# Optimization experiments

Hardware: AMD Instinct MI355X
Metric: run time of the kernel (lower is better)

The kernel has to match this reference:

```python
import jax, jax.numpy as jnp
import numpy as np

T, N, E, D = 6, 50000, 250000, 256   # edge types, nodes/type, edges/type, feat dim
H, C, K = 4, 64, 64                  # heads, head dim, diffpool clusters (H*C == D)
SCALE = 0.06


def setup_inputs():
    key = jax.random.key(0)
    ks = jax.random.split(key, 14)
    return {
        'x_pkg': jax.random.normal(ks[0], (N, D), jnp.float32),
        'x_dst': jax.random.normal(ks[1], (T, N, D), jnp.float32),
        'edge_index': jax.random.randint(ks[2], (T, 2, E), 0, N, jnp.int32),
        'edge_attr': jax.random.uniform(ks[3], (T, E, 1), jnp.float32),
        'node_mask': jnp.ones((N,), jnp.float32),
        'edge_mask': jax.random.uniform(ks[4], (E,), jnp.float32),
        'W1_src': jax.random.normal(ks[5], (T, D, H, C), jnp.float32) * SCALE,
        'W1_dst': jax.random.normal(ks[6], (T, D, H, C), jnp.float32) * SCALE,
        'a1': jax.random.normal(ks[7], (T, H, C), jnp.float32) * SCALE,
        'W2_src': jax.random.normal(ks[8], (T, D, H, C), jnp.float32) * SCALE,
        'W2_dst': jax.random.normal(ks[9], (T, D, H, C), jnp.float32) * SCALE,
        'a2': jax.random.normal(ks[10], (T, H, C), jnp.float32) * SCALE,
        'W_assign': jax.random.normal(ks[11], (D, K), jnp.float32) * SCALE,
        'W_cls': jax.random.normal(ks[12], (D + T, 1), jnp.float32) * SCALE,
        'b_cls': jnp.zeros((1,), jnp.float32),
    }


def _gatv2(x_src, x_dst, src, dst, Ws, Wd, a, edge_w):
    """GATv2Conv (bipartite, no self loops) with soft edge-mask weighting."""
    hs = jnp.einsum('nd,dhc->nhc', x_src, Ws)          # [N,H,C]
    hd = jnp.einsum('nd,dhc->nhc', x_dst, Wd)          # [N,H,C]
    hj = hs[src]                                        # [E,H,C] gathered source msgs
    e = jnp.sum(a * jax.nn.leaky_relu(hd[dst] + hj, 0.2), axis=-1)  # [E,H]
    m = jax.ops.segment_max(e, dst, num_segments=N)
    m = jnp.where(jnp.isfinite(m), m, 0.0)              # nodes with no in-edges
    p = jnp.exp(e - m[dst])
    den = jax.ops.segment_sum(p, dst, num_segments=N)
    alpha = p / (den[dst] + 1e-16)                      # softmax over in-neighbors
    msg = (alpha * edge_w[:, None])[:, :, None] * hj    # [E,H,C]
    return jax.ops.segment_sum(msg, dst, num_segments=N).reshape(N, H * C)


def reference(x_pkg, x_dst, edge_index, edge_attr, node_mask, edge_mask,
              W1_src, W1_dst, a1, W2_src, W2_dst, a2, W_assign, W_cls, b_cls):
    nm = node_mask[:, None]
    xm_pkg = x_pkg * nm
    # layer 1: hetero GATv2 per edge type (Package_Name -> dst type)
    h1 = [
        _gatv2(xm_pkg, x_dst[t] * nm, edge_index[t, 0], edge_index[t, 1],
               W1_src[t], W1_dst[t], a1[t], edge_mask)
        for t in range(T)
    ]
    # layer 2 on relu'd features (H*C == D so dims line up)
    x2_src = jax.nn.relu(x_pkg)
    h2 = [
        _gatv2(x2_src, jax.nn.relu(h1[t]), edge_index[t, 0], edge_index[t, 1],
               W2_src[t], W2_dst[t], a2[t], edge_mask)
        for t in range(T)
    ]
    # diffpool on last processed node type
    x_last = h2[-1]                                     # [N, D]
    S = jax.nn.softmax(x_last @ W_assign, axis=-1)      # [N, K] cluster assignment
    x_pool = S.T @ x_last                               # [K, D]
    # global aggregated edge features (mean per edge type)
    agg_edge = jnp.concatenate([edge_attr[t].mean(axis=0) for t in range(T)], -1)  # [T]
    feats = jnp.concatenate([x_pool, jnp.broadcast_to(agg_edge, (K, T))], axis=-1)
    logits = feats @ W_cls + b_cls                      # [K, 1]
    return jax.nn.sigmoid(logits)
```

## Files before the change

kernel.cpp:

```cpp
#include <hip/hip_runtime.h>
#include <math.h>

#define NN 50000
#define EE 250000
#define TTT 6
#define DD 256
#define HH 4
#define CC 64
#define KDIM 64

typedef __bf16 bf16x4 __attribute__((ext_vector_type(4)));
typedef __bf16 bf16x8 __attribute__((ext_vector_type(8)));
typedef float  f32x4  __attribute__((ext_vector_type(4)));

__device__ __forceinline__ void mfma_bf16(f32x4& d, bf16x8 a, bf16x8 b) {
    asm("v_mfma_f32_16x16x32_bf16 %0, %1, %2, %0" : "+v"(d) : "v"(a), "v"(b));
}

__global__ __launch_bounds__(256) void prep_b_k(
    const float* __restrict__ B0, const float* __restrict__ B1,
    const float* __restrict__ B2, const float* __restrict__ B3,
    __bf16* __restrict__ outp)
{
    int w = blockIdx.y;
    const float* B = (w == 0) ? B0 : (w == 1) ? B1 : (w == 2) ? B2 : B3;
    __bf16* oh = outp + (size_t)w * 2 * DD * DD;
    __bf16* ol = oh + DD * DD;
    int i = blockIdx.x * 256 + threadIdx.x;
    int k = i >> 8, n = i & 255;
    float x = B[i];
    __bf16 h = (__bf16)x;
    __bf16 l = (__bf16)(x - (float)h);
    oh[(size_t)n * DD + k] = h;
    ol[(size_t)n * DD + k] = l;
}

#define BM 128
#define BN 128
#define BK 64

__global__ __launch_bounds__(256, 2) void gemm_mfma_k(
    const float* __restrict__ A, const __bf16* __restrict__ Bt,
    float* __restrict__ Cout, const float* __restrict__ rowscale,
    int op, int nrows)
{
    __shared__ __align__(16) __bf16 Ah[BM * BK], Al[BM * BK];
    __shared__ __align__(16) __bf16 Bh[BN * BK], Bl[BN * BK];
    const __bf16* Bth = Bt;
    const __bf16* Btl = Bt + DD * DD;
    int tid = threadIdx.x;
    int row0 = blockIdx.x * BM;
    int col0 = blockIdx.y * BN;
    int lane = tid & 63;
    int wv = tid >> 6;
    int wm = (wv >> 1) * 64;
    int wn = (wv & 1) * 64;
    f32x4 acc[4][4] = {};

    for (int k0 = 0; k0 < DD; k0 += BK) {
        #pragma unroll
        for (int li = 0; li < 8; ++li) {
            int i = tid + li * 256;
            int r = i >> 4;
            int kq = (i & 15) * 4;
            int gr = row0 + r;
            float4 v = make_float4(0.f, 0.f, 0.f, 0.f);
            if (gr < nrows) {
                v = *(const float4*)&A[(size_t)gr * DD + k0 + kq];
                if (op == 0) {
                    float s = rowscale[gr];
                    v.x *= s; v.y *= s; v.z *= s; v.w *= s;
                } else {
                    v.x = fmaxf(v.x, 0.f); v.y = fmaxf(v.y, 0.f);
                    v.z = fmaxf(v.z, 0.f); v.w = fmaxf(v.w, 0.f);
                }
            }
            bf16x4 hv, lv;
            hv[0] = (__bf16)v.x; hv[1] = (__bf16)v.y;
            hv[2] = (__bf16)v.z; hv[3] = (__bf16)v.w;
            lv[0] = (__bf16)(v.x - (float)hv[0]);
            lv[1] = (__bf16)(v.y - (float)hv[1]);
            lv[2] = (__bf16)(v.z - (float)hv[2]);
            lv[3] = (__bf16)(v.w - (float)hv[3]);
            int kk = kq ^ ((r & 7) << 3);
            *(bf16x4*)&Ah[r * BK + kk] = hv;
            *(bf16x4*)&Al[r * BK + kk] = lv;
        }
        #pragma unroll
        for (int li = 0; li < 4; ++li) {
            int i = tid + li * 256;
            int r = i >> 3;
            int kc = (i & 7) * 8;
            int kk = kc ^ ((r & 7) << 3);
            *(bf16x8*)&Bh[r * BK + kk] = *(const bf16x8*)&Bth[(size_t)(col0 + r) * DD + k0 + kc];
            *(bf16x8*)&Bl[r * BK + kk] = *(const bf16x8*)&Btl[(size_t)(col0 + r) * DD + k0 + kc];
        }
        __syncthreads();
        #pragma unroll
        for (int ks = 0; ks < 2; ++ks) {
            bf16x8 af[4], alf[4], bfr[4], blf[4];
            int kb = ks * 32 + (lane >> 4) * 8;
            #pragma unroll
            for (int i2 = 0; i2 < 4; ++i2) {
                int r = wm + i2 * 16 + (lane & 15);
                int kk = kb ^ ((r & 7) << 3);
                af[i2]  = *(const bf16x8*)&Ah[r * BK + kk];
                alf[i2] = *(const bf16x8*)&Al[r * BK + kk];
            }
            #pragma unroll
            for (int j = 0; j < 4; ++j) {
                int r = wn + j * 16 + (lane & 15);
                int kk = kb ^ ((r & 7) << 3);
                bfr[j] = *(const bf16x8*)&Bh[r * BK + kk];
                blf[j] = *(const bf16x8*)&Bl[r * BK + kk];
            }
            #pragma unroll
            for (int i2 = 0; i2 < 4; ++i2)
                #pragma unroll
                for (int j = 0; j < 4; ++j) {
                    mfma_bf16(acc[i2][j], af[i2],  bfr[j]);
                    mfma_bf16(acc[i2][j], af[i2],  blf[j]);
                    mfma_bf16(acc[i2][j], alf[i2], bfr[j]);
                }
        }
        __syncthreads();
    }
    #pragma unroll
    for (int i2 = 0; i2 < 4; ++i2) {
        int rbase = row0 + wm + i2 * 16 + (lane >> 4) * 4;
        #pragma unroll
        for (int rr = 0; rr < 4; ++rr) {
            int gr = rbase + rr;
            if (gr < nrows) {
                #pragma unroll
                for (int j = 0; j < 4; ++j)
                    Cout[(size_t)gr * DD + col0 + wn + j * 16 + (lane & 15)] = acc[i2][j][rr];
            }
        }
    }
}

__global__ __launch_bounds__(256) void count_k(const int* __restrict__ dst,
                                               int* __restrict__ deg, int nedges)
{
    int e = blockIdx.x * 256 + threadIdx.x;
    if (e < nedges) atomicAdd(&deg[dst[e]], 1);
}

__global__ __launch_bounds__(1024) void scan_k(const int* __restrict__ deg,
                                               int* __restrict__ offs)
{
    __shared__ int part[1024];
    int tid = threadIdx.x;
    const int CH = (NN + 1023) / 1024;
    int base = tid * CH;
    int s = 0;
    for (int i = 0; i < CH; ++i)
        if (base + i < NN) s += deg[base + i];
    part[tid] = s;
    __syncthreads();
    for (int off = 1; off < 1024; off <<= 1) {
        int v = (tid >= off) ? part[tid - off] : 0;
        __syncthreads();
        part[tid] += v;
        __syncthreads();
    }
    int run = part[tid] - s;
    for (int i = 0; i < CH; ++i) {
        if (base + i < NN) { offs[base + i] = run; run += deg[base + i]; }
    }
    if (tid == 1023) offs[NN] = part[1023];
}

__global__ __launch_bounds__(256) void scatter_k(const int* __restrict__ dst,
                                                 const int* __restrict__ offs,
                                                 int* __restrict__ cursor,
                                                 int* __restrict__ eord, int nedges)
{
    int e = blockIdx.x * 256 + threadIdx.x;
    if (e < nedges) {
        int d = dst[e];
        int p = atomicAdd(&cursor[d], 1);
        eord[offs[d] + p] = e;
    }
}

__global__ __launch_bounds__(256) void edge_fused_k(
    const float* __restrict__ hs, const float* __restrict__ hd,
    const int* __restrict__ src, const float* __restrict__ emask,
    const int* __restrict__ eord, const int* __restrict__ offs,
    const float* __restrict__ avec, float* __restrict__ hout)
{
    int lane = threadIdx.x & 63;
    int n = (int)((blockIdx.x * 256 + threadIdx.x) >> 6);
    if (n >= NN) return;
    int eslot = lane >> 4;
    int c16 = lane & 15;
    float hdv[HH][4], av[HH][4], accv[HH][4], den[HH];
    #pragma unroll
    for (int h = 0; h < HH; ++h) {
        float4 t = *(const float4*)&hd[(size_t)n * DD + h * CC + c16 * 4];
        hdv[h][0] = t.x; hdv[h][1] = t.y; hdv[h][2] = t.z; hdv[h][3] = t.w;
        float4 u = *(const float4*)&avec[h * CC + c16 * 4];
        av[h][0] = u.x; av[h][1] = u.y; av[h][2] = u.z; av[h][3] = u.w;
        accv[h][0] = accv[h][1] = accv[h][2] = accv[h][3] = 0.f;
        den[h] = 0.f;
    }
    int b = offs[n], e2 = offs[n + 1];
    for (int i0 = b; i0 < e2; i0 += 4) {
        int idx = i0 + eslot;
        bool valid = idx < e2;
        int idxc = valid ? idx : b;
        int e = eord[idxc];
        int s = src[e];
        float ew = emask[e];
        const float* prs = hs + (size_t)s * DD;
        float hsv[HH][4], v[HH];
        #pragma unroll
        for (int h = 0; h < HH; ++h) {
            float4 t = *(const float4*)&prs[h * CC + c16 * 4];
            hsv[h][0] = t.x; hsv[h][1] = t.y; hsv[h][2] = t.z; hsv[h][3] = t.w;
            float vv = 0.f;
            #pragma unroll
            for (int j = 0; j < 4; ++j) {
                float xx = hdv[h][j] + hsv[h][j];
                xx = xx > 0.f ? xx : 0.2f * xx;
                vv = fmaf(av[h][j], xx, vv);
            }
            v[h] = vv;
        }
        #pragma unroll
        for (int h = 0; h < HH; ++h) {
            float vv = v[h];
            #pragma unroll
            for (int off = 1; off < 16; off <<= 1) vv += __shfl_xor(vv, off, 64);
            float pf = valid ? expf(vv) : 0.f;
            den[h] += pf;
            float pw = pf * ew;
            #pragma unroll
            for (int j = 0; j < 4; ++j)
                accv[h][j] = fmaf(pw, hsv[h][j], accv[h][j]);
        }
    }
    #pragma unroll
    for (int h = 0; h < HH; ++h) {
        den[h] += __shfl_xor(den[h], 16, 64);
        den[h] += __shfl_xor(den[h], 32, 64);
        #pragma unroll
        for (int j = 0; j < 4; ++j) {
            accv[h][j] += __shfl_xor(accv[h][j], 16, 64);
            accv[h][j] += __shfl_xor(accv[h][j], 32, 64);
        }
    }
    if (eslot == 0) {
        #pragma unroll
        for (int h = 0; h < HH; ++h) {
            float r = 1.f / (den[h] + 1e-16f);
            float4 o = { accv[h][0] * r, accv[h][1] * r, accv[h][2] * r, accv[h][3] * r };
            *(float4*)&hout[(size_t)n * DD + h * CC + c16 * 4] = o;
        }
    }
}

#define MBLK 120
__global__ __launch_bounds__(256) void edge_mean1_k(
    const float* __restrict__ eattr, double* __restrict__ partial, int nedges)
{
    __shared__ double sh[256];
    int tid = threadIdx.x;
    int stride = MBLK * 256;
    #pragma unroll
    for (int t = 0; t < TTT; ++t) {
        double a = 0.0;
        for (int i = blockIdx.x * 256 + tid; i < nedges; i += stride)
            a += (double)eattr[(size_t)t * nedges + i];
        sh[tid] = a;
        __syncthreads();
        #pragma unroll
        for (int s = 128; s; s >>= 1) {
            if (tid < s) sh[tid] += sh[tid + s];
            __syncthreads();
        }
        if (tid == 0) partial[(size_t)blockIdx.x * TTT + t] = sh[0];
        __syncthreads();
    }
}

#define AM 64
#define AK 32
__global__ __launch_bounds__(256) void assign_reduce_k(
    const float* __restrict__ x, const float* __restrict__ Wa,
    const float* __restrict__ wcls, float* __restrict__ logit_acc, int nrows)
{
    __shared__ __align__(16) float As[AK][AM + 4];
    __shared__ __align__(16) float Bs[AK][KDIM];
    __shared__ float wc[DD];
    __shared__ float Ps[AM][KDIM + 1];
    __shared__ float zp[4][AM];
    __shared__ float zsh[AM], rs[AM];
    int tid = threadIdx.x;
    int row0 = blockIdx.x * AM;
    int tx = tid & 15, ty = tid >> 4;
    for (int i = tid; i < DD; i += 256) wc[i] = wcls[i];
    float acc[4][4] = {};
    float zacc = 0.f;
    int node = tid & 63, part = tid >> 6;
    for (int k0 = 0; k0 < DD; k0 += AK) {
        for (int i = tid; i < AM * AK; i += 256) {
            int r = i / AK, k = i % AK;
            int gr = row0 + r;
            As[k][r] = (gr < nrows) ? x[(size_t)gr * DD + k0 + k] : 0.f;
        }
        for (int i = tid; i < AK * KDIM; i += 256) {
            int k = i >> 6, m = i & 63;
            Bs[k][m] = Wa[(size_t)(k0 + k) * KDIM + m];
        }
        __syncthreads();
        #pragma unroll
        for (int kk = 0; kk < AK; ++kk) {
            float4 a4 = *(const float4*)&As[kk][ty * 4];
            float4 b4 = *(const float4*)&Bs[kk][tx * 4];
            float av[4] = {a4.x, a4.y, a4.z, a4.w};
            float bv[4] = {b4.x, b4.y, b4.z, b4.w};
            #pragma unroll
            for (int i2 = 0; i2 < 4; ++i2)
                #pragma unroll
                for (int j = 0; j < 4; ++j)
                    acc[i2][j] = fmaf(av[i2], bv[j], acc[i2][j]);
        }
        #pragma unroll
        for (int kk = part * 8; kk < part * 8 + 8; ++kk)
            zacc = fmaf(As[kk][node], wc[k0 + kk], zacc);
        __syncthreads();
    }
    #pragma unroll
    for (int i2 = 0; i2 < 4; ++i2)
        #pragma unroll
        for (int j = 0; j < 4; ++j)
            Ps[ty * 4 + i2][tx * 4 + j] = acc[i2][j];
    zp[part][node] = zacc;
    __syncthreads();
    if (tid < AM) {
        float z = zp[0][tid] + zp[1][tid] + zp[2][tid] + zp[3][tid];
        zsh[tid] = z;
        float m = -1e30f;
        for (int k = 0; k < KDIM; ++k) m = fmaxf(m, Ps[tid][k]);
        float s = 0.f;
        for (int k = 0; k < KDIM; ++k) {
            float v = expf(Ps[tid][k] - m);
            Ps[tid][k] = v;
            s += v;
        }
        rs[tid] = s;
    }
    __syncthreads();
    if (tid < KDIM) {
        float t = 0.f;
        for (int n = 0; n < AM; ++n)
            t += Ps[n][tid] / rs[n] * zsh[n];
        atomicAdd(&logit_acc[tid], t);
    }
}

__global__ void final_k(const float* __restrict__ logit, const double* __restrict__ partial,
                        const float* __restrict__ Wcls, const float* __restrict__ bcls,
                        float* __restrict__ out)
{
    int k = threadIdx.x;
    double acc = (double)logit[k];
    #pragma unroll
    for (int t = 0; t < TTT; ++t) {
        double s = 0.0;
        for (int b = 0; b < MBLK; ++b) s += partial[(size_t)b * TTT + t];
        acc += (s / (double)EE) * (double)Wcls[DD + t];
    }
    acc += (double)bcls[0];
    out[k] = (float)(1.0 / (1.0 + exp(-acc)));
}

extern "C" void kernel_launch(void* const* d_in, const int* in_sizes, int n_in,
                              void* d_out, int out_size, void* d_ws, size_t ws_size,
                              hipStream_t stream)
{
    const float* x_pkg   = (const float*)d_in[0];
    const float* x_dst   = (const float*)d_in[1];
    const int*   eindex  = (const int*)d_in[2];
    const float* eattr   = (const float*)d_in[3];
    const float* nmask   = (const float*)d_in[4];
    const float* emask   = (const float*)d_in[5];
    const float* W1s     = (const float*)d_in[6];
    const float* W1d     = (const float*)d_in[7];
    const float* a1      = (const float*)d_in[8];
    const float* W2s     = (const float*)d_in[9];
    const float* W2d     = (const float*)d_in[10];
    const float* a2      = (const float*)d_in[11];
    const float* Wassign = (const float*)d_in[12];
    const float* Wcls    = (const float*)d_in[13];
    const float* bcls    = (const float*)d_in[14];
    float* out = (float*)d_out;

    const int t = TTT - 1;
    const int* src5 = eindex + (size_t)t * 2 * EE;
    const int* dst5 = src5 + EE;
    const float* xdst5 = x_dst + (size_t)t * NN * DD;
    const float* W1s5 = W1s + (size_t)t * DD * HH * CC;
    const float* W1d5 = W1d + (size_t)t * DD * HH * CC;
    const float* a15  = a1 + (size_t)t * HH * CC;
    const float* W2s5 = W2s + (size_t)t * DD * HH * CC;
    const float* W2d5 = W2d + (size_t)t * DD * HH * CC;
    const float* a25  = a2 + (size_t)t * HH * CC;

    char* wsb = (char*)d_ws;
    size_t off = 0;
    auto carve = [&](size_t bytes) -> void* {
        void* p = wsb + off;
        off += (bytes + 255) & ~(size_t)255;
        return p;
    };
    float* hs     = (float*)carve((size_t)NN * DD * sizeof(float));
    float* hd     = (float*)carve((size_t)NN * DD * sizeof(float));
    float* hbuf   = (float*)carve((size_t)NN * DD * sizeof(float));
    int*   deg    = (int*)carve((size_t)NN * sizeof(int));
    int*   cursor = (int*)carve((size_t)NN * sizeof(int));
    int*   offs   = (int*)carve((size_t)(NN + 1) * sizeof(int));
    int*   eord   = (int*)carve((size_t)EE * sizeof(int));
    float* logit  = (float*)carve(KDIM * sizeof(float));
    double* partial = (double*)carve((size_t)MBLK * TTT * sizeof(double));
    __bf16* bprep = (__bf16*)carve((size_t)4 * 2 * DD * DD * sizeof(__bf16));

    dim3 ggrid((NN + BM - 1) / BM, DD / BN);
    int edge_node_blocks = (NN + 3) / 4;
    int eb = (EE + 255) / 256;

    hipMemsetAsync(deg, 0, (size_t)NN * sizeof(int), stream);
    hipMemsetAsync(cursor, 0, (size_t)NN * sizeof(int), stream);
    hipMemsetAsync(logit, 0, KDIM * sizeof(float), stream);

    prep_b_k<<<dim3(256, 4), 256, 0, stream>>>(W1s5, W1d5, W2s5, W2d5, bprep);
    edge_mean1_k<<<MBLK, 256, 0, stream>>>(eattr, partial, EE);
    count_k<<<eb, 256, 0, stream>>>(dst5, deg, EE);
    scan_k<<<1, 1024, 0, stream>>>(deg, offs);
    scatter_k<<<eb, 256, 0, stream>>>(dst5, offs, cursor, eord, EE);

    gemm_mfma_k<<<ggrid, 256, 0, stream>>>(x_pkg, bprep + 0 * 2 * DD * DD, hs, nmask, 0, NN);
    gemm_mfma_k<<<ggrid, 256, 0, stream>>>(xdst5, bprep + 1 * 2 * DD * DD, hd, nmask, 0, NN);
    edge_fused_k<<<edge_node_blocks, 256, 0, stream>>>(hs, hd, src5, emask, eord, offs, a15, hbuf);

    gemm_mfma_k<<<ggrid, 256, 0, stream>>>(hbuf, bprep + 3 * 2 * DD * DD, hd, nullptr, 1, NN);
    gemm_mfma_k<<<ggrid, 256, 0, stream>>>(x_pkg, bprep + 2 * 2 * DD * DD, hs, nullptr, 1, NN);
    edge_fused_k<<<edge_node_blocks, 256, 0, stream>>>(hs, hd, src5, emask, eord, offs, a25, hbuf);

    assign_reduce_k<<<(NN + AM - 1) / AM, 256, 0, stream>>>(hbuf, Wassign, Wcls, logit, NN);
    final_k<<<1, KDIM, 0, stream>>>(logit, partial, Wcls, bcls, out);
}
```

Measured before the change: 964.4 us.

## Store projected features in bf16, batch paired GEMMs via grid z, merge memsets

The GEMM outputs hs/hd are now written as bf16 instead of fp32, and the edge kernel reads them as bf16x4 and converts to float. This halves the bytes of the random source-row gathers and of the GEMM stores. The two independent projections at each layer are launched as one kernel using blockIdx.z to pick operands, and three memsets are merged into one contiguous span. The cost is reduced precision in the attention logits and messages.

```diff
diff --git a/kernel.cpp b/kernel.cpp
--- a/kernel.cpp
+++ b/kernel.cpp
@@ -40,14 +40,18 @@
 #define BK 64
 
 __global__ __launch_bounds__(256, 2) void gemm_mfma_k(
-    const float* __restrict__ A, const __bf16* __restrict__ Bt,
-    float* __restrict__ Cout, const float* __restrict__ rowscale,
+    const float* __restrict__ A0, const float* __restrict__ A1,
+    const __bf16* __restrict__ Bt0, const __bf16* __restrict__ Bt1,
+    __bf16* __restrict__ C0, __bf16* __restrict__ C1,
+    const float* __restrict__ rowscale,
     int op, int nrows)
 {
     __shared__ __align__(16) __bf16 Ah[BM * BK], Al[BM * BK];
     __shared__ __align__(16) __bf16 Bh[BN * BK], Bl[BN * BK];
-    const __bf16* Bth = Bt;
-    const __bf16* Btl = Bt + DD * DD;
+    const float*  A    = blockIdx.z ? A1 : A0;
+    const __bf16* Bth  = blockIdx.z ? Bt1 : Bt0;
+    const __bf16* Btl  = Bth + DD * DD;
+    __bf16*       Cout = blockIdx.z ? C1 : C0;
     int tid = threadIdx.x;
     int row0 = blockIdx.x * BM;
     int col0 = blockIdx.y * BN;
@@ -134,7 +138,7 @@
             if (gr < nrows) {
                 #pragma unroll
                 for (int j = 0; j < 4; ++j)
-                    Cout[(size_t)gr * DD + col0 + wn + j * 16 + (lane & 15)] = acc[i2][j][rr];
+                    Cout[(size_t)gr * DD + col0 + wn + j * 16 + (lane & 15)] = (__bf16)acc[i2][j][rr];
             }
         }
     }
@@ -186,7 +190,7 @@
 }
 
 __global__ __launch_bounds__(256) void edge_fused_k(
-    const float* __restrict__ hs, const float* __restrict__ hd,
+    const __bf16* __restrict__ hs, const __bf16* __restrict__ hd,
     const int* __restrict__ src, const float* __restrict__ emask,
     const int* __restrict__ eord, const int* __restrict__ offs,
     const float* __restrict__ avec, float* __restrict__ hout)
@@ -199,8 +203,9 @@
     float hdv[HH][4], av[HH][4], accv[HH][4], den[HH];
     #pragma unroll
     for (int h = 0; h < HH; ++h) {
-        float4 t = *(const float4*)&hd[(size_t)n * DD + h * CC + c16 * 4];
-        hdv[h][0] = t.x; hdv[h][1] = t.y; hdv[h][2] = t.z; hdv[h][3] = t.w;
+        bf16x4 t = *(const bf16x4*)&hd[(size_t)n * DD + h * CC + c16 * 4];
+        hdv[h][0] = (float)t[0]; hdv[h][1] = (float)t[1];
+        hdv[h][2] = (float)t[2]; hdv[h][3] = (float)t[3];
         float4 u = *(const float4*)&avec[h * CC + c16 * 4];
         av[h][0] = u.x; av[h][1] = u.y; av[h][2] = u.z; av[h][3] = u.w;
         accv[h][0] = accv[h][1] = accv[h][2] = accv[h][3] = 0.f;
@@ -214,12 +219,13 @@
         int e = eord[idxc];
         int s = src[e];
         float ew = emask[e];
-        const float* prs = hs + (size_t)s * DD;
+        const __bf16* prs = hs + (size_t)s * DD;
         float hsv[HH][4], v[HH];
         #pragma unroll
         for (int h = 0; h < HH; ++h) {
-            float4 t = *(const float4*)&prs[h * CC + c16 * 4];
-            hsv[h][0] = t.x; hsv[h][1] = t.y; hsv[h][2] = t.z; hsv[h][3] = t.w;
+            bf16x4 t = *(const bf16x4*)&prs[h * CC + c16 * 4];
+            hsv[h][0] = (float)t[0]; hsv[h][1] = (float)t[1];
+            hsv[h][2] = (float)t[2]; hsv[h][3] = (float)t[3];
             float vv = 0.f;
             #pragma unroll
             for (int j = 0; j < 4; ++j) {
@@ -417,24 +423,23 @@
         off += (bytes + 255) & ~(size_t)255;
         return p;
     };
-    float* hs     = (float*)carve((size_t)NN * DD * sizeof(float));
-    float* hd     = (float*)carve((size_t)NN * DD * sizeof(float));
+    __bf16* hs    = (__bf16*)carve((size_t)NN * DD * sizeof(__bf16));
+    __bf16* hd    = (__bf16*)carve((size_t)NN * DD * sizeof(__bf16));
     float* hbuf   = (float*)carve((size_t)NN * DD * sizeof(float));
     int*   deg    = (int*)carve((size_t)NN * sizeof(int));
     int*   cursor = (int*)carve((size_t)NN * sizeof(int));
+    float* logit  = (float*)carve(KDIM * sizeof(float));
+    size_t zero_span = (size_t)(wsb + off) - (size_t)deg;
     int*   offs   = (int*)carve((size_t)(NN + 1) * sizeof(int));
     int*   eord   = (int*)carve((size_t)EE * sizeof(int));
-    float* logit  = (float*)carve(KDIM * sizeof(float));
     double* partial = (double*)carve((size_t)MBLK * TTT * sizeof(double));
     __bf16* bprep = (__bf16*)carve((size_t)4 * 2 * DD * DD * sizeof(__bf16));
 
-    dim3 ggrid((NN + BM - 1) / BM, DD / BN);
+    dim3 ggrid((NN + BM - 1) / BM, DD / BN, 2);
     int edge_node_blocks = (NN + 3) / 4;
     int eb = (EE + 255) / 256;
 
-    hipMemsetAsync(deg, 0, (size_t)NN * sizeof(int), stream);
-    hipMemsetAsync(cursor, 0, (size_t)NN * sizeof(int), stream);
-    hipMemsetAsync(logit, 0, KDIM * sizeof(float), stream);
+    hipMemsetAsync(deg, 0, zero_span, stream);
 
     prep_b_k<<<dim3(256, 4), 256, 0, stream>>>(W1s5, W1d5, W2s5, W2d5, bprep);
     edge_mean1_k<<<MBLK, 256, 0, stream>>>(eattr, partial, EE);
@@ -442,12 +447,16 @@
     scan_k<<<1, 1024, 0, stream>>>(deg, offs);
     scatter_k<<<eb, 256, 0, stream>>>(dst5, offs, cursor, eord, EE);
 
-    gemm_mfma_k<<<ggrid, 256, 0, stream>>>(x_pkg, bprep + 0 * 2 * DD * DD, hs, nmask, 0, NN);
-    gemm_mfma_k<<<ggrid, 256, 0, stream>>>(xdst5, bprep + 1 * 2 * DD * DD, hd, nmask, 0, NN);
+    gemm_mfma_k<<<ggrid, 256, 0, stream>>>(
+        x_pkg, xdst5,
+        bprep + 0 * 2 * DD * DD, bprep + 1 * 2 * DD * DD,
+        hs, hd, nmask, 0, NN);
     edge_fused_k<<<edge_node_blocks, 256, 0, stream>>>(hs, hd, src5, emask, eord, offs, a15, hbuf);
 
-    gemm_mfma_k<<<ggrid, 256, 0, stream>>>(hbuf, bprep + 3 * 2 * DD * DD, hd, nullptr, 1, NN);
-    gemm_mfma_k<<<ggrid, 256, 0, stream>>>(x_pkg, bprep + 2 * 2 * DD * DD, hs, nullptr, 1, NN);
+    gemm_mfma_k<<<ggrid, 256, 0, stream>>>(
+        hbuf, x_pkg,
+        bprep + 3 * 2 * DD * DD, bprep + 2 * 2 * DD * DD,
+        hd, hs, nullptr, 1, NN);
     edge_fused_k<<<edge_node_blocks, 256, 0, stream>>>(hs, hd, src5, emask, eord, offs, a25, hbuf);
 
     assign_reduce_k<<<(NN + AM - 1) / AM, 256, 0, stream>>>(hbuf, Wassign, Wcls, logit, NN);
```

Result: faster. 942.1 us (-2.3%).
